# Kernel tuning notes

Measured on AMD Instinct MI355X. Metric: run time of the kernel, lower is better.

The kernel has to match this reference:

```python
import jax, jax.numpy as jnp
import numpy as np

B, C, H, W = 4, 64, 160, 160
OUT, KH, KW = 64, 3, 3
STRIDE, PAD = 1, 1
K2 = KH * KW


def conv2d(x, w, b=None, stride=STRIDE, pad=PAD):
    y = jax.lax.conv_general_dilated(
        x, w, window_strides=(stride, stride),
        padding=[(pad, pad), (pad, pad)],
        dimension_numbers=("NCHW", "OIHW", "NCHW"))
    if b is not None:
        y = y + b[None, :, None, None]
    return y


def bilinear_gather(x, py, px):
    # x: [B,C,H,W]; py,px: [B,K2,Ho,Wo] float sampling positions
    Bq, Cq, Hq, Wq = x.shape
    y0 = jnp.floor(py)
    x0 = jnp.floor(px)
    wy1 = py - y0  # frac
    wx1 = px - x0
    y0i = y0.astype(jnp.int32)
    x0i = x0.astype(jnp.int32)
    x_flat = x.reshape(Bq, Cq, Hq * Wq)

    def corner(yi, xi, wgt):
        valid = (yi >= 0) & (yi < Hq) & (xi >= 0) & (xi < Wq)
        idx = jnp.clip(yi, 0, Hq - 1) * Wq + jnp.clip(xi, 0, Wq - 1)  # [B,K2,Ho,Wo]
        g = jax.vmap(lambda xf, i: jnp.take(xf, i, axis=1))(x_flat, idx)  # [B,C,K2,Ho,Wo]
        return g * (wgt * valid)[:, None]

    out = corner(y0i, x0i, (1 - wy1) * (1 - wx1))
    out = out + corner(y0i, x0i + 1, (1 - wy1) * wx1)
    out = out + corner(y0i + 1, x0i, wy1 * (1 - wx1))
    out = out + corner(y0i + 1, x0i + 1, wy1 * wx1)
    return out  # [B,C,K2,Ho,Wo]


def deform_forward(x, offset_w, offset_b, mask_w, mask_b, dcn_w):
    offset = conv2d(x, offset_w, offset_b)                # [B, 2*K2, Ho, Wo]
    mask = jax.nn.sigmoid(conv2d(x, mask_w, mask_b))      # [B, K2, Ho, Wo]
    Bq, _, Ho, Wo = offset.shape
    off = offset.reshape(Bq, K2, 2, Ho, Wo)
    off_y, off_x = off[:, :, 0], off[:, :, 1]
    k = jnp.arange(K2)
    ky = (k // KW).astype(jnp.float32)
    kx = (k % KW).astype(jnp.float32)
    base_i = jnp.arange(Ho, dtype=jnp.float32) * STRIDE - PAD
    base_j = jnp.arange(Wo, dtype=jnp.float32) * STRIDE - PAD
    py = off_y + base_i[None, None, :, None] + ky[None, :, None, None]
    px = off_x + base_j[None, None, None, :] + kx[None, :, None, None]
    sampled = bilinear_gather(x, py, px)                  # [B,C,K2,Ho,Wo]
    w = dcn_w.reshape(OUT, C, K2)
    # out[b,o,i,j] = sum_{c,k} w[o,c,k] * mask[b,k,i,j] * sampled[b,c,k,i,j]
    return jnp.einsum("ock,bckij,bkij->boij", w, sampled, mask)


def setup_inputs() -> dict:
    key = jax.random.key(0)
    ks = jax.random.split(key, 6)
    x = jax.random.normal(ks[0], (B, C, H, W), dtype=jnp.float32)
    # small random weights so offsets stay modest (module inits them to 0;
    # random values exercise the full deformable math)
    offset_w = jax.random.normal(ks[1], (2 * K2, C, KH, KW), dtype=jnp.float32) * 0.01
    offset_b = jax.random.normal(ks[2], (2 * K2,), dtype=jnp.float32) * 0.1
    mask_w = jax.random.normal(ks[3], (K2, C, KH, KW), dtype=jnp.float32) * 0.01
    mask_b = jax.random.normal(ks[4], (K2,), dtype=jnp.float32) * 0.1
    dcn_w = jax.random.normal(ks[5], (OUT, C, KH, KW), dtype=jnp.float32) * (1.0 / np.sqrt(C * K2))
    return {"x": x, "offset_w": offset_w, "offset_b": offset_b,
            "mask_w": mask_w, "mask_b": mask_b, "dcn_w": dcn_w}


def reference(x, offset_w, offset_b, mask_w, mask_b, dcn_w):
    return deform_forward(x, offset_w, offset_b, mask_w, mask_b, dcn_w)
```

## Files before the change

kernel.cpp:

```cpp
#include <hip/hip_runtime.h>
#include <hip/hip_bf16.h>
#include <math.h>

#define Bq 4
#define Cq 64
#define Hq 160
#define Wq 160
#define HWq (Hq*Wq)
#define OUTq 64
#define KKq 576
#define KS  18
#define SROW 584
#define HSTRIDE 72

typedef __attribute__((ext_vector_type(8))) short short8;
typedef __attribute__((ext_vector_type(4))) float float4v;
typedef __attribute__((ext_vector_type(2))) float float2v;
typedef unsigned short ushort_t;

__device__ __forceinline__ unsigned int f2bfu(float f) {
    unsigned int u = __builtin_bit_cast(unsigned int, f);
    unsigned int r = u + 0x7fffu + ((u >> 16) & 1u);
    return r >> 16;
}
__device__ __forceinline__ float bflo(unsigned int u) {
    return __builtin_bit_cast(float, u << 16);
}
__device__ __forceinline__ float bfhi(unsigned int u) {
    return __builtin_bit_cast(float, u & 0xffff0000u);
}

__global__ void __launch_bounds__(256) k_prep(const float* __restrict__ x,
                                              const float* __restrict__ dcn_w,
                                              const float* __restrict__ off_w,
                                              const float* __restrict__ msk_w,
                                              ushort_t* __restrict__ xt,
                                              ushort_t* __restrict__ wtf,
                                              ushort_t* __restrict__ cwf2) {
    __shared__ float tile[64][65];
    int b = blockIdx.y, hw0 = blockIdx.x * 64;
    int tid = threadIdx.x;
    int lane = tid & 63, grp = tid >> 6;
#pragma unroll
    for (int i = 0; i < 16; ++i) {
        int c = grp*16 + i;
        tile[c][lane] = x[(b*Cq + c)*HWq + hw0 + lane];
    }
    __syncthreads();
    int cp = tid & 31, hwg = tid >> 5;
#pragma unroll
    for (int it = 0; it < 8; ++it) {
        int hw = it*8 + hwg;
        unsigned int v = f2bfu(tile[2*cp][hw]) | (f2bfu(tile[2*cp+1][hw]) << 16);
        *(unsigned int*)(xt + ((size_t)b*HWq + hw0 + hw)*64 + 2*cp) = v;
    }
    if (blockIdx.y == 0 && blockIdx.x < 216) {
        int id = blockIdx.x*256 + tid;
        if (id < 4*KS*512) {
            int j = id & 7, ln = (id>>3) & 63, ks = (id>>9) % KS, g = id/(512*KS);
            int kk = ks*32 + (ln>>4)*8 + j;
            int c  = kk & 63, kt = kk >> 6;
            int m  = g*16 + (ln&15);
            wtf[id] = (ushort_t)f2bfu(dcn_w[m*KKq + c*9 + kt]);
        }
        int id2 = id - 4*KS*512;
        if (id2 >= 0 && id2 < 9*2*2*512) {
            int j = id2 & 7, ln = (id2>>3) & 63;
            int ks2 = (id2>>9) & 1, g = (id2>>10) & 1, k = id2 >> 11;
            int co = g*16 + (ln&15);
            int c  = ks2*32 + (ln>>4)*8 + j;
            float w = 0.f;
            if (co < 18)      w = off_w[co*KKq + c*9 + k];
            else if (co < 27) w = msk_w[(co-18)*KKq + c*9 + k];
            cwf2[id2] = (ushort_t)f2bfu(w);
        }
    }
}

__global__ void __launch_bounds__(256, 7) k_fused(const ushort_t* __restrict__ xt,
                                                  const ushort_t* __restrict__ cwf2,
                                                  const float* __restrict__ off_b,
                                                  const float* __restrict__ msk_b,
                                                  const ushort_t* __restrict__ wtf,
                                                  float* __restrict__ out) {
    __shared__ __align__(16) char s_mem[16*SROW*2];
    __shared__ __align__(16) uint4  s_A[144];
    __shared__ __align__(16) float4 s_W[144];
    ushort_t* halo   = (ushort_t*)s_mem;
    float*    s_part = (float*)(s_mem + 7776);
    ushort_t* s_s    = (ushort_t*)s_mem;

    int blk = blockIdx.x;
    int jt = blk % 10, i = (blk/10) % Hq, b = blk/(10*Hq);
    int j0 = jt*16;
    int tid = threadIdx.x, lane = tid & 63, grp = tid >> 6;
    int n = lane & 15, quad = lane >> 4;

    const ushort_t* xtb = xt + (size_t)b*HWq*64;
    for (int t = tid; t < 432; t += 256) {
        int seg = t >> 3, sub = t & 7;
        int ky = seg / 18, px = seg % 18;
        int y = i + ky - 1, xx = j0 + px - 1;
        uint4 v = {0u,0u,0u,0u};
        if (y >= 0 && y < Hq && xx >= 0 && xx < Wq)
            v = *(const uint4*)(xtb + ((size_t)y*Wq + xx)*64 + sub*8);
        *(uint4*)(halo + (ky*18 + px)*HSTRIDE + sub*8) = v;
    }
    __syncthreads();

    {
        int gM = grp & 1, kh = grp >> 1;
        float4v cacc = {0.f,0.f,0.f,0.f};
#pragma unroll
        for (int s = 0; s < 9; ++s) {
            int st = kh*9 + s;
            int k = st >> 1, ks2 = st & 1;
            int ky = k/3, kx = k - (k/3)*3;
            short8 a  = *(const short8*)(cwf2 + (size_t)(((k*2+gM)*2+ks2)*512 + lane*8));
            short8 bf = *(const short8*)(halo + (ky*18 + n + kx)*HSTRIDE + quad*8 + ks2*32);
            cacc = __builtin_amdgcn_mfma_f32_16x16x32_bf16(a, bf, cacc, 0, 0, 0);
        }
        *(float4v*)(s_part + grp*256 + lane*4) = cacc;
    }
    __syncthreads();

    if (tid < 144) {
        int p = tid & 15, k = tid >> 4;
        #define RD(co) (s_part[(((co)>>4)*256)     + ((((co)&15)>>2)*16 + p)*4 + ((co)&3)] + \
                        s_part[(2 + ((co)>>4))*256 + ((((co)&15)>>2)*16 + p)*4 + ((co)&3)])
        float oy = RD(2*k)   + off_b[2*k];
        float ox = RD(2*k+1) + off_b[2*k+1];
        float mv = RD(18+k)  + msk_b[k];
        #undef RD
        float m = 1.f/(1.f + __expf(-mv));
        float py = oy + (float)(i - 1 + k/3);
        float px = ox + (float)(j0 + p - 1 + (k - (k/3)*3));
        float fy = floorf(py), fx = floorf(px);
        int y0 = (int)fy, x0 = (int)fx;
        float wy1 = py - fy, wx1 = px - fx;
        float wy0 = 1.f - wy1, wx0 = 1.f - wx1;
        bool vy0 = (y0 >= 0) & (y0 < Hq),   vy1 = (y0+1 >= 0) & (y0+1 < Hq);
        bool vx0 = (x0 >= 0) & (x0 < Wq),   vx1 = (x0+1 >= 0) & (x0+1 < Wq);
        int yc0 = min(max(y0,   0), Hq-1), yc1 = min(max(y0+1, 0), Hq-1);
        int xc0 = min(max(x0,   0), Wq-1), xc1 = min(max(x0+1, 0), Wq-1);
        s_A[tid] = make_uint4((unsigned int)((yc0*Wq + xc0)*128),
                              (unsigned int)((yc0*Wq + xc1)*128),
                              (unsigned int)((yc1*Wq + xc0)*128),
                              (unsigned int)((yc1*Wq + xc1)*128));
        s_W[tid] = make_float4((vy0 && vx0) ? wy0*wx0*m : 0.f,
                               (vy0 && vx1) ? wy0*wx1*m : 0.f,
                               (vy1 && vx0) ? wy1*wx0*m : 0.f,
                               (vy1 && vx1) ? wy1*wx1*m : 0.f);
    }
    __syncthreads();

    {
        int lane4 = (lane & 31) * 4;
        int halfi = lane >> 5;
        const char* xtbB = (const char*)xtb;
        char* s_sb = (char*)s_s;
#pragma unroll 2
        for (int iter = 0; iter < 18; ++iter) {
            int t2h = iter*8 + grp*2 + halfi;
            uint4  A  = s_A[t2h];
            float4 Wt = s_W[t2h];
            unsigned int dst = (unsigned int)((t2h & 15)*(SROW*2) + (t2h >> 4)*128);
            unsigned int u00 = *(const unsigned int*)(xtbB + A.x + lane4);
            unsigned int u01 = *(const unsigned int*)(xtbB + A.y + lane4);
            unsigned int u10 = *(const unsigned int*)(xtbB + A.z + lane4);
            unsigned int u11 = *(const unsigned int*)(xtbB + A.w + lane4);
            float2v v00 = {bflo(u00), bfhi(u00)};
            float2v v01 = {bflo(u01), bfhi(u01)};
            float2v v10 = {bflo(u10), bfhi(u10)};
            float2v v11 = {bflo(u11), bfhi(u11)};
            float2v s2 = v00 * Wt.x;
            s2 += v01 * Wt.y;
            s2 += v10 * Wt.z;
            s2 += v11 * Wt.w;
            __hip_bfloat162 h2 = __float22bfloat162_rn(make_float2(s2.x, s2.y));
            *(__hip_bfloat162*)(s_sb + dst + lane4) = h2;
        }
    }
    __syncthreads();

    float4v acc = {0.f,0.f,0.f,0.f};
    const ushort_t* arow = wtf + ((size_t)(grp*KS)*64 + lane)*8;
    const ushort_t* brow = s_s + n*SROW + quad*8;
#pragma unroll
    for (int ks = 0; ks < KS; ++ks) {
        short8 a  = *(const short8*)(arow + ks*512);
        short8 bf = *(const short8*)(brow + ks*32);
        acc = __builtin_amdgcn_mfma_f32_16x16x32_bf16(a, bf, acc, 0, 0, 0);
    }

#pragma unroll
    for (int r = 0; r < 4; ++r) {
        int o = grp*16 + quad*4 + r;
        out[(((size_t)b*OUTq + o)*Hq + i)*Wq + j0 + n] = acc[r];
    }
}

extern "C" void kernel_launch(void* const* d_in, const int* in_sizes, int n_in,
                              void* d_out, int out_size, void* d_ws, size_t ws_size,
                              hipStream_t stream) {
    const float* x     = (const float*)d_in[0];
    const float* off_w = (const float*)d_in[1];
    const float* off_b = (const float*)d_in[2];
    const float* msk_w = (const float*)d_in[3];
    const float* msk_b = (const float*)d_in[4];
    const float* dcn_w = (const float*)d_in[5];
    float* out = (float*)d_out;

    char* ws = (char*)d_ws;
    ushort_t* xt   = (ushort_t*)ws;
    ushort_t* wtf  = xt + (size_t)Bq*HWq*64;
    ushort_t* cwf2 = wtf + 4*KS*512;

    hipLaunchKernelGGL(k_prep, dim3(HWq/64, Bq), dim3(256), 0, stream,
                       x, dcn_w, off_w, msk_w, xt, wtf, cwf2);
    hipLaunchKernelGGL(k_fused, dim3(Bq*Hq*10), dim3(256), 0, stream,
                       xt, cwf2, off_b, msk_b, wtf, out);
}
```

Before: 135.5 us.

## Tile four output rows per block and gather bilinear samples directly into MFMA registers

New measurement: 164.4 us. 1.21x slower.

```diff
diff --git a/kernel.cpp b/kernel.cpp
--- a/kernel.cpp
+++ b/kernel.cpp
@@ -10,13 +10,13 @@
 #define OUTq 64
 #define KKq 576
 #define KS  18
-#define SROW 584
 #define HSTRIDE 72
 
 typedef __attribute__((ext_vector_type(8))) short short8;
 typedef __attribute__((ext_vector_type(4))) float float4v;
 typedef __attribute__((ext_vector_type(2))) float float2v;
 typedef unsigned short ushort_t;
+typedef unsigned int uint_t;
 
 __device__ __forceinline__ unsigned int f2bfu(float f) {
     unsigned int u = __builtin_bit_cast(unsigned int, f);
@@ -29,6 +29,13 @@
 __device__ __forceinline__ float bfhi(unsigned int u) {
     return __builtin_bit_cast(float, u & 0xffff0000u);
 }
+__device__ __forceinline__ uint_t packbf(float a, float b) {
+    return f2bfu(a) | (f2bfu(b) << 16);
+}
+__device__ __forceinline__ uint_t pkbf2(float2v v) {
+    return f2bfu(v.x) | (f2bfu(v.y) << 16);
+}
+#define MFMA(a,b,c) __builtin_amdgcn_mfma_f32_16x16x32_bf16((a),(b),(c),0,0,0)
 
 __global__ void __launch_bounds__(256) k_prep(const float* __restrict__ x,
                                               const float* __restrict__ dcn_w,
@@ -77,64 +84,68 @@
     }
 }
 
-__global__ void __launch_bounds__(256, 7) k_fused(const ushort_t* __restrict__ xt,
+__global__ void __launch_bounds__(256, 6) k_fused(const ushort_t* __restrict__ xt,
                                                   const ushort_t* __restrict__ cwf2,
                                                   const float* __restrict__ off_b,
                                                   const float* __restrict__ msk_b,
                                                   const ushort_t* __restrict__ wtf,
                                                   float* __restrict__ out) {
-    __shared__ __align__(16) char s_mem[16*SROW*2];
-    __shared__ __align__(16) uint4  s_A[144];
-    __shared__ __align__(16) float4 s_W[144];
-    ushort_t* halo   = (ushort_t*)s_mem;
-    float*    s_part = (float*)(s_mem + 7776);
-    ushort_t* s_s    = (ushort_t*)s_mem;
-
-    int blk = blockIdx.x;
-    int jt = blk % 10, i = (blk/10) % Hq, b = blk/(10*Hq);
-    int j0 = jt*16;
-    int tid = threadIdx.x, lane = tid & 63, grp = tid >> 6;
+    __shared__ __align__(16) char s_halo[6*18*HSTRIDE*2];
+    __shared__ __align__(16) float s_part[4*2*64*4];
+
+    int m = blockIdx.x;
+    int blk = (m & 7)*200 + (m >> 3);
+    int jt = blk % 10, it = (blk/10) % 40, b = blk/400;
+    int i0 = it*4, j0 = jt*16;
+    int tid = threadIdx.x, lane = tid & 63, w = tid >> 6;
     int n = lane & 15, quad = lane >> 4;
 
     const ushort_t* xtb = xt + (size_t)b*HWq*64;
-    for (int t = tid; t < 432; t += 256) {
+    ushort_t* halo = (ushort_t*)s_halo;
+
+    for (int t = tid; t < 864; t += 256) {
         int seg = t >> 3, sub = t & 7;
-        int ky = seg / 18, px = seg % 18;
-        int y = i + ky - 1, xx = j0 + px - 1;
+        int ry = seg / 18, px = seg % 18;
+        int y = i0 + ry - 1, xx = j0 + px - 1;
         uint4 v = {0u,0u,0u,0u};
         if (y >= 0 && y < Hq && xx >= 0 && xx < Wq)
             v = *(const uint4*)(xtb + ((size_t)y*Wq + xx)*64 + sub*8);
-        *(uint4*)(halo + (ky*18 + px)*HSTRIDE + sub*8) = v;
+        *(uint4*)(halo + (ry*18 + px)*HSTRIDE + sub*8) = v;
     }
     __syncthreads();
 
     {
-        int gM = grp & 1, kh = grp >> 1;
-        float4v cacc = {0.f,0.f,0.f,0.f};
-#pragma unroll
-        for (int s = 0; s < 9; ++s) {
-            int st = kh*9 + s;
-            int k = st >> 1, ks2 = st & 1;
+        float4v c0 = {0.f,0.f,0.f,0.f}, c1 = {0.f,0.f,0.f,0.f};
+#pragma unroll
+        for (int k = 0; k < 9; ++k) {
             int ky = k/3, kx = k - (k/3)*3;
-            short8 a  = *(const short8*)(cwf2 + (size_t)(((k*2+gM)*2+ks2)*512 + lane*8));
-            short8 bf = *(const short8*)(halo + (ky*18 + n + kx)*HSTRIDE + quad*8 + ks2*32);
-            cacc = __builtin_amdgcn_mfma_f32_16x16x32_bf16(a, bf, cacc, 0, 0, 0);
-        }
-        *(float4v*)(s_part + grp*256 + lane*4) = cacc;
-    }
-    __syncthreads();
-
-    if (tid < 144) {
-        int p = tid & 15, k = tid >> 4;
-        #define RD(co) (s_part[(((co)>>4)*256)     + ((((co)&15)>>2)*16 + p)*4 + ((co)&3)] + \
-                        s_part[(2 + ((co)>>4))*256 + ((((co)&15)>>2)*16 + p)*4 + ((co)&3)])
+            const ushort_t* bb = halo + ((w + ky)*18 + n + kx)*HSTRIDE + quad*8;
+#pragma unroll
+            for (int ks2 = 0; ks2 < 2; ++ks2) {
+                short8 bf = *(const short8*)(bb + ks2*32);
+                short8 a0 = *(const short8*)(cwf2 + (size_t)(((k*2+0)*2+ks2)*512 + lane*8));
+                short8 a1 = *(const short8*)(cwf2 + (size_t)(((k*2+1)*2+ks2)*512 + lane*8));
+                c0 = MFMA(a0, bf, c0);
+                c1 = MFMA(a1, bf, c1);
+            }
+        }
+        *(float4v*)(s_part + ((w*2+0)*64 + lane)*4) = c0;
+        *(float4v*)(s_part + ((w*2+1)*64 + lane)*4) = c1;
+    }
+    __syncthreads();
+
+    uint4* desc = (uint4*)s_halo;
+    for (int t = tid; t < 576; t += 256) {
+        int p = t & 63, k = t >> 6;
+        int pw = p >> 4, pn = p & 15;
+        #define RD(co) s_part[((pw*2 + ((co)>>4))*64 + (((co)&15)>>2)*16 + pn)*4 + ((co)&3)]
         float oy = RD(2*k)   + off_b[2*k];
         float ox = RD(2*k+1) + off_b[2*k+1];
         float mv = RD(18+k)  + msk_b[k];
         #undef RD
-        float m = 1.f/(1.f + __expf(-mv));
-        float py = oy + (float)(i - 1 + k/3);
-        float px = ox + (float)(j0 + p - 1 + (k - (k/3)*3));
+        float mk = 1.f/(1.f + __expf(-mv));
+        float py = oy + (float)(i0 + pw - 1 + k/3);
+        float px = ox + (float)(j0 + pn - 1 + (k - (k/3)*3));
         float fy = floorf(py), fx = floorf(px);
         int y0 = (int)fy, x0 = (int)fx;
         float wy1 = py - fy, wx1 = px - fx;
@@ -143,60 +154,77 @@
         bool vx0 = (x0 >= 0) & (x0 < Wq),   vx1 = (x0+1 >= 0) & (x0+1 < Wq);
         int yc0 = min(max(y0,   0), Hq-1), yc1 = min(max(y0+1, 0), Hq-1);
         int xc0 = min(max(x0,   0), Wq-1), xc1 = min(max(x0+1, 0), Wq-1);
-        s_A[tid] = make_uint4((unsigned int)((yc0*Wq + xc0)*128),
-                              (unsigned int)((yc0*Wq + xc1)*128),
-                              (unsigned int)((yc1*Wq + xc0)*128),
-                              (unsigned int)((yc1*Wq + xc1)*128));
-        s_W[tid] = make_float4((vy0 && vx0) ? wy0*wx0*m : 0.f,
-                               (vy0 && vx1) ? wy0*wx1*m : 0.f,
-                               (vy1 && vx0) ? wy1*wx0*m : 0.f,
-                               (vy1 && vx1) ? wy1*wx1*m : 0.f);
-    }
-    __syncthreads();
-
-    {
-        int lane4 = (lane & 31) * 4;
-        int halfi = lane >> 5;
-        const char* xtbB = (const char*)xtb;
-        char* s_sb = (char*)s_s;
-#pragma unroll 2
-        for (int iter = 0; iter < 18; ++iter) {
-            int t2h = iter*8 + grp*2 + halfi;
-            uint4  A  = s_A[t2h];
-            float4 Wt = s_W[t2h];
-            unsigned int dst = (unsigned int)((t2h & 15)*(SROW*2) + (t2h >> 4)*128);
-            unsigned int u00 = *(const unsigned int*)(xtbB + A.x + lane4);
-            unsigned int u01 = *(const unsigned int*)(xtbB + A.y + lane4);
-            unsigned int u10 = *(const unsigned int*)(xtbB + A.z + lane4);
-            unsigned int u11 = *(const unsigned int*)(xtbB + A.w + lane4);
-            float2v v00 = {bflo(u00), bfhi(u00)};
-            float2v v01 = {bflo(u01), bfhi(u01)};
-            float2v v10 = {bflo(u10), bfhi(u10)};
-            float2v v11 = {bflo(u11), bfhi(u11)};
-            float2v s2 = v00 * Wt.x;
-            s2 += v01 * Wt.y;
-            s2 += v10 * Wt.z;
-            s2 += v11 * Wt.w;
-            __hip_bfloat162 h2 = __float22bfloat162_rn(make_float2(s2.x, s2.y));
-            *(__hip_bfloat162*)(s_sb + dst + lane4) = h2;
-        }
-    }
-    __syncthreads();
-
-    float4v acc = {0.f,0.f,0.f,0.f};
-    const ushort_t* arow = wtf + ((size_t)(grp*KS)*64 + lane)*8;
-    const ushort_t* brow = s_s + n*SROW + quad*8;
-#pragma unroll
-    for (int ks = 0; ks < KS; ++ks) {
-        short8 a  = *(const short8*)(arow + ks*512);
-        short8 bf = *(const short8*)(brow + ks*32);
-        acc = __builtin_amdgcn_mfma_f32_16x16x32_bf16(a, bf, acc, 0, 0, 0);
-    }
-
-#pragma unroll
-    for (int r = 0; r < 4; ++r) {
-        int o = grp*16 + quad*4 + r;
-        out[(((size_t)b*OUTq + o)*Hq + i)*Wq + j0 + n] = acc[r];
+        uint_t i00 = (uint_t)(yc0*Wq + xc0), i01 = (uint_t)(yc0*Wq + xc1);
+        uint_t i10 = (uint_t)(yc1*Wq + xc0), i11 = (uint_t)(yc1*Wq + xc1);
+        float w00 = (vy0 && vx0) ? wy0*wx0*mk : 0.f;
+        float w01 = (vy0 && vx1) ? wy0*wx1*mk : 0.f;
+        float w10 = (vy1 && vx0) ? wy1*wx0*mk : 0.f;
+        float w11 = (vy1 && vx1) ? wy1*wx1*mk : 0.f;
+        desc[p*9 + k] = make_uint4(i00 | (i01 << 16), i10 | (i11 << 16),
+                                   packbf(w00, w01), packbf(w10, w11));
+    }
+    __syncthreads();
+
+    int i = i0 + w;
+    const char* xtc = (const char*)xtb;
+    const char* wtc = (const char*)wtf;
+    float4v acc[4] = {{0.f,0.f,0.f,0.f},{0.f,0.f,0.f,0.f},
+                      {0.f,0.f,0.f,0.f},{0.f,0.f,0.f,0.f}};
+    uint_t qoff = (uint_t)(quad*16);
+    uint_t aoffb = (uint_t)(lane*16);
+#pragma unroll
+    for (int k = 0; k < 9; ++k) {
+        uint4 d = desc[(w*16 + n)*9 + k];
+        uint_t vo00 = ((d.x & 0xffffu) << 7) + qoff;
+        uint_t vo01 = ((d.x >> 16)     << 7) + qoff;
+        uint_t vo10 = ((d.y & 0xffffu) << 7) + qoff;
+        uint_t vo11 = ((d.y >> 16)     << 7) + qoff;
+        float w00 = bflo(d.z), w01 = bfhi(d.z);
+        float w10 = bflo(d.w), w11 = bfhi(d.w);
+#pragma unroll
+        for (int ks2 = 0; ks2 < 2; ++ks2) {
+            int ks = k*2 + ks2;
+            uint4 u00 = *(const uint4*)(xtc + vo00 + ks2*64);
+            uint4 u01 = *(const uint4*)(xtc + vo01 + ks2*64);
+            uint4 u10 = *(const uint4*)(xtc + vo10 + ks2*64);
+            uint4 u11 = *(const uint4*)(xtc + vo11 + ks2*64);
+            float2v q0 = (float2v){bflo(u00.x), bfhi(u00.x)} * w00;
+            float2v q1 = (float2v){bflo(u00.y), bfhi(u00.y)} * w00;
+            float2v q2 = (float2v){bflo(u00.z), bfhi(u00.z)} * w00;
+            float2v q3 = (float2v){bflo(u00.w), bfhi(u00.w)} * w00;
+            q0 += (float2v){bflo(u01.x), bfhi(u01.x)} * w01;
+            q1 += (float2v){bflo(u01.y), bfhi(u01.y)} * w01;
+            q2 += (float2v){bflo(u01.z), bfhi(u01.z)} * w01;
+            q3 += (float2v){bflo(u01.w), bfhi(u01.w)} * w01;
+            q0 += (float2v){bflo(u10.x), bfhi(u10.x)} * w10;
+            q1 += (float2v){bflo(u10.y), bfhi(u10.y)} * w10;
+            q2 += (float2v){bflo(u10.z), bfhi(u10.z)} * w10;
+            q3 += (float2v){bflo(u10.w), bfhi(u10.w)} * w10;
+            q0 += (float2v){bflo(u11.x), bfhi(u11.x)} * w11;
+            q1 += (float2v){bflo(u11.y), bfhi(u11.y)} * w11;
+            q2 += (float2v){bflo(u11.z), bfhi(u11.z)} * w11;
+            q3 += (float2v){bflo(u11.w), bfhi(u11.w)} * w11;
+            uint4 br = make_uint4(pkbf2(q0), pkbf2(q1), pkbf2(q2), pkbf2(q3));
+            short8 bfr = __builtin_bit_cast(short8, br);
+            uint_t ao = (uint_t)(ks*1024) + aoffb;
+            short8 a0 = *(const short8*)(wtc + ao);
+            short8 a1 = *(const short8*)(wtc + 18432 + ao);
+            short8 a2 = *(const short8*)(wtc + 36864 + ao);
+            short8 a3 = *(const short8*)(wtc + 55296 + ao);
+            acc[0] = MFMA(a0, bfr, acc[0]);
+            acc[1] = MFMA(a1, bfr, acc[1]);
+            acc[2] = MFMA(a2, bfr, acc[2]);
+            acc[3] = MFMA(a3, bfr, acc[3]);
+        }
+    }
+
+#pragma unroll
+    for (int mt = 0; mt < 4; ++mt) {
+#pragma unroll
+        for (int r = 0; r < 4; ++r) {
+            int o = mt*16 + quad*4 + r;
+            out[(((size_t)b*OUTq + o)*Hq + i)*Wq + j0 + n] = acc[mt][r];
+        }
     }
 }
 
@@ -218,6 +246,6 @@
 
     hipLaunchKernelGGL(k_prep, dim3(HWq/64, Bq), dim3(256), 0, stream,
                        x, dcn_w, off_w, msk_w, xt, wtf, cwf2);
-    hipLaunchKernelGGL(k_fused, dim3(Bq*Hq*10), dim3(256), 0, stream,
+    hipLaunchKernelGGL(k_fused, dim3(1600), dim3(256), 0, stream,
                        xt, cwf2, off_b, msk_b, wtf, out);
 }
```
